# Kernel optimization log

Measured on AMD Instinct MI355X. Metric: run time of the kernel, lower is better.

## Reference

```python
import jax, jax.numpy as jnp
import numpy as np

B, S, D, H = 4, 2048, 1024, 16
HD = D // H  # 64

def setup_inputs() -> dict:
    key = jax.random.key(0)
    ks = jax.random.split(key, 6)
    scale = 1.0 / np.sqrt(D)
    return {
        "x": jax.random.normal(ks[0], (B, S, D), dtype=jnp.float32),
        "Wq": jax.random.normal(ks[1], (D, D), dtype=jnp.float32) * scale,
        "Wk": jax.random.normal(ks[2], (D, D), dtype=jnp.float32) * scale,
        "Wv": jax.random.normal(ks[3], (D, D), dtype=jnp.float32) * scale,
        "Wo": jax.random.normal(ks[4], (D, D), dtype=jnp.float32) * scale,
        "bo": jnp.zeros((D,), dtype=jnp.float32),
    }

def reference(x, Wq, Wk, Wv, Wo, bo):
    b, s, d = x.shape
    # projections (no bias for q/k/v, matching QKV_BIAS=False)
    q = (x @ Wq).reshape(b, s, H, HD).transpose(0, 2, 1, 3)  # [b,h,s,hd]
    k = (x @ Wk).reshape(b, s, H, HD).transpose(0, 2, 1, 3)
    v = (x @ Wv).reshape(b, s, H, HD).transpose(0, 2, 1, 3)
    scores = jnp.einsum('bhqd,bhkd->bhqk', q, k)  # [b,h,s,s]
    causal = jnp.tril(jnp.ones((s, s), dtype=bool))  # True where allowed
    scores = jnp.where(causal, scores, -jnp.inf)
    attn = jax.nn.softmax(scores / np.sqrt(HD), axis=-1)
    ctx = jnp.einsum('bhqk,bhkd->bhqd', attn, v)  # [b,h,s,hd]
    ctx = ctx.transpose(0, 2, 1, 3).reshape(b, s, d)
    return ctx @ Wo + bo
```

## Files before the change

kernel.cpp:

```cpp
#include <hip/hip_runtime.h>

#define BSZ 4
#define SEQ 2048
#define DIM 1024
#define NH  16
#define HD  64
#define QT  128
#define KT  64
#define PAD 72

typedef float v4f __attribute__((ext_vector_type(4)));
typedef short s8v __attribute__((ext_vector_type(8)));
typedef unsigned short u16;
typedef unsigned short u16x8 __attribute__((ext_vector_type(8)));
typedef unsigned short u16x4 __attribute__((ext_vector_type(4)));
typedef unsigned int u32;
typedef unsigned int u32x2 __attribute__((ext_vector_type(2)));
typedef unsigned int u32x4 __attribute__((ext_vector_type(4)));

__device__ __forceinline__ u16 f2bf(float f) {
  u32 u = __builtin_bit_cast(u32, f);
  u32 r = u + 0x7fffu + ((u >> 16) & 1u);
  return (u16)(r >> 16);
}
__device__ __forceinline__ u32 cvtpk(float lo, float hi) {
  u32 r; asm("v_cvt_pk_bf16_f32 %0, %1, %2" : "=v"(r) : "v"(lo), "v"(hi)); return r;
}
__device__ __forceinline__ u16 f2bf1(float f) { return (u16)cvtpk(f, f); }
__device__ __forceinline__ float fast_exp2(float x) {
#if __has_builtin(__builtin_amdgcn_exp2f)
  return __builtin_amdgcn_exp2f(x);
#else
  return exp2f(x);
#endif
}
__device__ __forceinline__ void gll16(const u16* g, u16* l) {
  __builtin_amdgcn_global_load_lds((const __attribute__((address_space(1))) void*)g,
                                   (__attribute__((address_space(3))) void*)l, 16, 0, 0);
}
__device__ __forceinline__ void wg_barrier() { asm volatile("s_barrier" ::: "memory"); }
#define WAITCNT_LGKM0 0xC07F
#define VMW8 __builtin_amdgcn_s_waitcnt(0xF78);
#define VMW6 __builtin_amdgcn_s_waitcnt(0xF76);
#define VMW4 __builtin_amdgcn_s_waitcnt(0xF74);
#define VMW0 __builtin_amdgcn_s_waitcnt(0xF70);
#define SCHEDB __builtin_amdgcn_sched_barrier(0);

__global__ __launch_bounds__(256) void cast_bf16_kernel(const float* __restrict__ x,
                                                        u16* __restrict__ o, int n4) {
  int i = blockIdx.x * 256 + threadIdx.x;
  if (i >= n4) return;
  v4f v = reinterpret_cast<const v4f*>(x)[i];
  u16x4 r;
  #pragma unroll
  for (int c = 0; c < 4; c++) r[c] = f2bf(v[c]);
  reinterpret_cast<u16x4*>(o)[i] = r;
}

__global__ __launch_bounds__(256) void transpose_cast_kernel(const float* __restrict__ W0,
                                                             const float* __restrict__ W1,
                                                             const float* __restrict__ W2,
                                                             const float* __restrict__ W3,
                                                             u16* __restrict__ out) {
  const float* W = blockIdx.z == 0 ? W0 : blockIdx.z == 1 ? W1 : blockIdx.z == 2 ? W2 : W3;
  const float scale = (blockIdx.z == 0) ? 0.18033688011112042f : 1.0f;
  u16* T = out + (size_t)blockIdx.z * DIM * DIM;
  __shared__ float tile[32][33];
  int tx = threadIdx.x & 31, ty = threadIdx.x >> 5;
  int bn = blockIdx.x * 32, bk = blockIdx.y * 32;
  #pragma unroll
  for (int r = 0; r < 4; r++) {
    int k = bk + ty + r * 8;
    tile[ty + r * 8][tx] = W[(size_t)k * DIM + bn + tx];
  }
  __syncthreads();
  #pragma unroll
  for (int r = 0; r < 4; r++) {
    int n = bn + ty + r * 8;
    T[(size_t)n * DIM + bk + tx] = f2bf(tile[tx][ty + r * 8] * scale);
  }
}


#define QST_A(t_, kc_, d_)                                                        \
  gll16(AgLo + (t_) * 64 + (kc_) * 32, ALw + (d_) * 16384 + (kc_) * 8192);        \
  gll16(AgHi + (t_) * 64 + (kc_) * 32, ALw + (d_) * 16384 + (kc_) * 8192 + 4096);
#define QST_B(t_, kc_, d_)                                                        \
  gll16(BgLo + (t_) * 64 + (kc_) * 32, BLw + (d_) * 16384 + (kc_) * 8192);        \
  gll16(BgHi + (t_) * 64 + (kc_) * 32, BLw + (d_) * 16384 + (kc_) * 8192 + 4096);

#define QRDB(d_, kc_)                                                             \
  bfr[0] = *(const s8v*)(BL + (d_) * 16384 + (kc_) * 8192 + (wn * 4 + 0) * 512 + rdo); \
  bfr[1] = *(const s8v*)(BL + (d_) * 16384 + (kc_) * 8192 + (wn * 4 + 1) * 512 + rdo); \
  bfr[2] = *(const s8v*)(BL + (d_) * 16384 + (kc_) * 8192 + (wn * 4 + 2) * 512 + rdo); \
  bfr[3] = *(const s8v*)(BL + (d_) * 16384 + (kc_) * 8192 + (wn * 4 + 3) * 512 + rdo);

#define QPH(d_, kc_, mh_, RDB_, STG_, VMW_)                                       \
  { _Pragma("unroll") for (int i_ = 0; i_ < 4; i_++)                              \
      afr[i_] = *(const s8v*)(AL + (d_) * 16384 + (kc_) * 8192 +                  \
                              (wm * 8 + (mh_) * 4 + i_) * 512 + rdo);             \
    RDB_                                                                          \
    STG_                                                                          \
    SCHEDB                                                                        \
    VMW_                                                                          \
    wg_barrier();                                                                 \
    __builtin_amdgcn_s_waitcnt(WAITCNT_LGKM0);                                    \
    SCHEDB                                                                        \
    __builtin_amdgcn_s_setprio(1);                                                \
    _Pragma("unroll") for (int i_ = 0; i_ < 4; i_++)                              \
      _Pragma("unroll") for (int j_ = 0; j_ < 4; j_++)                            \
        acc[(mh_) * 4 + i_][j_] = __builtin_amdgcn_mfma_f32_16x16x32_bf16(        \
            afr[i_], bfr[j_], acc[(mh_) * 4 + i_][j_], 0, 0, 0);                  \
    __builtin_amdgcn_s_setprio(0);                                                \
    wg_barrier(); }

__global__ __launch_bounds__(512, 2) void gemm_qkv(const u16* __restrict__ A, const u16* __restrict__ Wt,
                                                   u16* __restrict__ Qb, u16* __restrict__ Kb,
                                                   u16* __restrict__ Vtg) {
  const int bid = blockIdx.x;
  const int swz = (bid & 7) * 48 + (bid >> 3);
  const int z = swz >> 7;
  const int rem = swz & 127;
  const int m0 = (rem >> 2) * 256;
  const int n0 = (rem & 3) * 256;
  const u16* Bt = Wt + (size_t)z * DIM * DIM;

  extern __shared__ __align__(16) u16 lds[];
  const int t = threadIdx.x;
  const int lane = t & 63, w = t >> 6;
  const int wm = w >> 2, wn = w & 3;
  const int quad = lane >> 4, l16 = lane & 15;
  const int sR = lane & 15, sC = lane >> 4;
  u16* AL = lds;
  u16* BL = lds + 32768;
  u16* ALw = AL + w * 512;
  u16* BLw = BL + w * 512;
  const int rdo = quad * 128 + l16 * 8;
  const u16* AgLo = A + (size_t)(m0 + w * 16 + sR) * DIM + sC * 8;
  const u16* AgHi = AgLo + (size_t)128 * DIM;
  const u16* BgLo = Bt + (size_t)(n0 + w * 16 + sR) * DIM + sC * 8;
  const u16* BgHi = BgLo + (size_t)128 * DIM;

  v4f acc[8][4];
  #pragma unroll
  for (int i = 0; i < 8; i++)
    #pragma unroll
    for (int j = 0; j < 4; j++) acc[i][j] = (v4f){0.f, 0.f, 0.f, 0.f};
  s8v afr[4], bfr[4];

  QST_A(0, 0, 0) QST_B(0, 0, 0) QST_A(0, 1, 0) QST_B(0, 1, 0)
  QST_A(1, 0, 1) QST_B(1, 0, 1)
  SCHEDB
  VMW8
  wg_barrier();

  for (int it = 0; it < 7; ++it) {
    const int kt = it * 2;
    QPH(0, 0, 0, QRDB(0, 0), QST_A(kt + 1, 1, 1), )
    QPH(0, 0, 1, ,           QST_B(kt + 1, 1, 1), VMW6)
    QPH(0, 1, 0, QRDB(0, 1), QST_A(kt + 2, 0, 0), )
    QPH(0, 1, 1, ,           QST_B(kt + 2, 0, 0), VMW6)
    QPH(1, 0, 0, QRDB(1, 0), QST_A(kt + 2, 1, 0), )
    QPH(1, 0, 1, ,           QST_B(kt + 2, 1, 0), VMW6)
    QPH(1, 1, 0, QRDB(1, 1), QST_A(kt + 3, 0, 1), )
    QPH(1, 1, 1, ,           QST_B(kt + 3, 0, 1), VMW6)
  }
  QPH(0, 0, 0, QRDB(0, 0), QST_A(15, 1, 1), )
  QPH(0, 0, 1, ,           QST_B(15, 1, 1), VMW6)
  QPH(0, 1, 0, QRDB(0, 1), , )
  QPH(0, 1, 1, ,           , VMW4)
  QPH(1, 0, 0, QRDB(1, 0), , )
  QPH(1, 0, 1, ,           , VMW0)
  QPH(1, 1, 0, QRDB(1, 1), , )
  QPH(1, 1, 1, ,           , )

  if (z == 2) {
    #pragma unroll
    for (int mi = 0; mi < 8; mi++) {
      #pragma unroll
      for (int ni = 0; ni < 4; ni++) {
        int gm0 = m0 + wm * 128 + mi * 16 + quad * 4;
        int gn = n0 + wn * 64 + ni * 16 + l16;
        int b = gm0 >> 11, s0 = gm0 & (SEQ - 1), hh = gn >> 6, d = gn & (HD - 1);
        u32x2 pw;
        pw[0] = cvtpk(acc[mi][ni][0], acc[mi][ni][1]);
        pw[1] = cvtpk(acc[mi][ni][2], acc[mi][ni][3]);
        *(u16x4*)(Vtg + ((size_t)(b * NH + hh) * HD + d) * SEQ + s0) =
            __builtin_bit_cast(u16x4, pw);
      }
    }
  } else {
    u16* C = (z == 0) ? Qb : Kb;
    #pragma unroll
    for (int mi = 0; mi < 8; mi++) {
      #pragma unroll
      for (int ni = 0; ni < 4; ni++) {
        int gn = n0 + wn * 64 + ni * 16 + l16;
        #pragma unroll
        for (int r = 0; r < 4; r++) {
          int gm = m0 + wm * 128 + mi * 16 + quad * 4 + r;
          C[(size_t)gm * DIM + gn] = f2bf1(acc[mi][ni][r]);
        }
      }
    }
  }
}

#define ST_TILE(t_, s_)                                                           \
  gll16(Ag0 + (t_) * 64,      AW0 + (s_) * 16384);                                \
  gll16(Ag1 + (t_) * 64,      AW1 + (s_) * 16384);                                \
  gll16(Ag0 + (t_) * 64 + 32, AW0 + (s_) * 16384 + 8192);                         \
  gll16(Ag1 + (t_) * 64 + 32, AW1 + (s_) * 16384 + 8192);                         \
  gll16(Bg0 + (t_) * 64,      BW0 + (s_) * 8192);                                 \
  gll16(Bg0 + (t_) * 64 + 32, BW0 + (s_) * 8192 + 4096);

#define PH(t_, s_, STAGES, VMW)                                                   \
  { const u16* Ab = AL + (s_) * 16384 + aRd;                                      \
    const u16* Bb = BL + (s_) * 8192 + bRd;                                       \
    s8v af[2][4], bf[2][4];                                                       \
    _Pragma("unroll") for (int kc_ = 0; kc_ < 2; kc_++) {                         \
      _Pragma("unroll") for (int i_ = 0; i_ < 4; i_++)                            \
        af[kc_][i_] = *(const s8v*)(Ab + kc_ * 8192 + i_ * 512);                  \
      _Pragma("unroll") for (int j_ = 0; j_ < 4; j_++)                            \
        bf[kc_][j_] = *(const s8v*)(Bb + kc_ * 4096 + j_ * 512);                  \
    }                                                                             \
    STAGES                                                                        \
    VMW                                                                           \
    wg_barrier();                                                                 \
    __builtin_amdgcn_s_waitcnt(WAITCNT_LGKM0);                                    \
    __builtin_amdgcn_s_setprio(1);                                                \
    _Pragma("unroll") for (int kc_ = 0; kc_ < 2; kc_++)                           \
      _Pragma("unroll") for (int i_ = 0; i_ < 4; i_++)                            \
        _Pragma("unroll") for (int j_ = 0; j_ < 4; j_++)                          \
          acc[i_][j_] = __builtin_amdgcn_mfma_f32_16x16x32_bf16(                  \
              af[kc_][i_], bf[kc_][j_], acc[i_][j_], 0, 0, 0);                    \
    __builtin_amdgcn_s_setprio(0);                                                \
    wg_barrier(); }

__global__ __launch_bounds__(512, 2) void gemm_proj(const u16* __restrict__ A, const u16* __restrict__ Bt,
                                                    float* __restrict__ Cf, const float* __restrict__ bias) {
  const int bid = blockIdx.x;
  const int swz = (bid & 7) * 32 + (bid >> 3);
  const int m0 = (swz >> 3) * 256;
  const int n0 = (swz & 7) * 128;
  extern __shared__ __align__(16) u16 lds[];
  const int t = threadIdx.x;
  const int lane = t & 63, w = t >> 6;
  const int waveM = w >> 1, waveN = w & 1;
  const int quad = lane >> 4, l16 = lane & 15;
  const int sR = lane & 15, sC = lane >> 4;
  u16* AL = lds;
  u16* BL = lds + 49152;
  v4f acc[4][4];
  #pragma unroll
  for (int i = 0; i < 4; i++)
    #pragma unroll
    for (int j = 0; j < 4; j++) acc[i][j] = (v4f){0.f, 0.f, 0.f, 0.f};
  const u16* Ag0 = A + (size_t)(m0 + w * 32 + sR) * DIM + sC * 8;
  const u16* Ag1 = Ag0 + 16 * DIM;
  const u16* Bg0 = Bt + (size_t)(n0 + w * 16 + sR) * DIM + sC * 8;
  u16* AW0 = AL + w * 1024;
  u16* AW1 = AL + w * 1024 + 512;
  u16* BW0 = BL + w * 512;
  const int aRd = waveM * 2048 + quad * 128 + l16 * 8;
  const int bRd = waveN * 2048 + quad * 128 + l16 * 8;
  ST_TILE(0, 0) ST_TILE(1, 1)
  VMW6
  wg_barrier();
  #pragma unroll
  for (int t3 = 0; t3 < 12; t3 += 3) {
    PH(t3 + 0, 0, ST_TILE(t3 + 2, 2), VMW6)
    PH(t3 + 1, 1, ST_TILE(t3 + 3, 0), VMW6)
    PH(t3 + 2, 2, ST_TILE(t3 + 4, 1), VMW6)
  }
  PH(12, 0, ST_TILE(14, 2), VMW6)
  PH(13, 1, ST_TILE(15, 0), VMW6)
  PH(14, 2, , VMW0)
  PH(15, 0, , )
  #pragma unroll
  for (int ni = 0; ni < 4; ni++) {
    int gn = n0 + waveN * 64 + ni * 16 + l16;
    float bv = bias[gn];
    #pragma unroll
    for (int mi = 0; mi < 4; mi++) {
      #pragma unroll
      for (int r = 0; r < 4; r++) {
        int gm = m0 + waveM * 64 + mi * 16 + quad * 4 + r;
        Cf[(size_t)gm * DIM + gn] = acc[mi][ni][r] + bv;
      }
    }
  }
}

__global__ __launch_bounds__(256, 3) void flash_attn_mfma(const u16* __restrict__ Qb,
                                                          const u16* __restrict__ Kb,
                                                          const u16* __restrict__ Vtg,
                                                          u16* __restrict__ Ob) {
  const int h = blockIdx.x, px = blockIdx.y, bb = blockIdx.z;
  const int t = threadIdx.x;
  const int lane = t & 63, w = t >> 6;
  const int quad = lane >> 4, l16 = lane & 15;

  __shared__ u16 QPs[QT * PAD];
  __shared__ u16 Ks[KT * PAD];
  __shared__ u16 Vs[HD * PAD];

  const size_t qkbase = (size_t)bb * SEQ * DIM + h * HD;
  const size_t vbase = ((size_t)bb * NH + h) * (size_t)HD * SEQ;

  const int vrow = t >> 2, scol = (t & 3) * 16;
  const int krow = ((vrow >> 5) + 2 * ((vrow >> 2) & 1)) * 16 + ((vrow >> 3) & 3) * 4 + (vrow & 3);

  for (int pass = 0; pass < 2; pass++) {
    const int qi = (pass == 0) ? px : (SEQ / QT - 1 - px);
    const int q0 = qi * QT;
    const int wq = q0 + w * 32;
    const int ntiles = 2 * qi + 2;

    __syncthreads();

    {
      const int r = t >> 1, c0 = (t & 1) * 32;
      const u16* src = Qb + qkbase + (size_t)(q0 + r) * DIM + c0;
      #pragma unroll
      for (int ch = 0; ch < 4; ch++)
        *(u16x8*)(QPs + r * PAD + c0 + ch * 8) = *(const u16x8*)(src + ch * 8);
    }
    __syncthreads();

    s8v qf[2][2];
    #pragma unroll
    for (int ni = 0; ni < 2; ni++)
      #pragma unroll
      for (int kc = 0; kc < 2; kc++)
        qf[ni][kc] = *(const s8v*)(QPs + (w * 32 + ni * 16 + l16) * PAD + kc * 32 + quad * 8);

    u16x8 kr0, kr1, vr0, vr1;
    {
      const u16* kp = Kb + qkbase + (size_t)vrow * DIM + scol;
      kr0 = *(const u16x8*)kp; kr1 = *(const u16x8*)(kp + 8);
      const u16* vp = Vtg + vbase + (size_t)vrow * SEQ + scol;
      vr0 = *(const u16x8*)vp; vr1 = *(const u16x8*)(vp + 8);
    }

    float mrun[2] = {-1e30f, -1e30f}, lrun[2] = {0.f, 0.f};
    v4f O[4][2];
    #pragma unroll
    for (int di = 0; di < 4; di++)
      #pragma unroll
      for (int ni = 0; ni < 2; ni++) O[di][ni] = (v4f){0.f, 0.f, 0.f, 0.f};

    for (int it = 0; it < ntiles; ++it) {
      const int kv0 = it * KT;
      __syncthreads();
      *(u16x8*)(Ks + krow * PAD + scol) = kr0;
      *(u16x8*)(Ks + krow * PAD + scol + 8) = kr1;
      *(u16x8*)(Vs + vrow * PAD + scol) = vr0;
      *(u16x8*)(Vs + vrow * PAD + scol + 8) = vr1;
      __syncthreads();
      if (it + 1 < ntiles) {
        const int nkv = kv0 + KT;
        const u16* kp = Kb + qkbase + (size_t)(nkv + vrow) * DIM + scol;
        kr0 = *(const u16x8*)kp; kr1 = *(const u16x8*)(kp + 8);
        const u16* vp = Vtg + vbase + (size_t)vrow * SEQ + nkv + scol;
        vr0 = *(const u16x8*)vp; vr1 = *(const u16x8*)(vp + 8);
      }
      if (kv0 > wq + 31) continue;

      v4f sc[4][2];
      #pragma unroll
      for (int mi = 0; mi < 4; mi++)
        #pragma unroll
        for (int ni = 0; ni < 2; ni++) sc[mi][ni] = (v4f){0.f, 0.f, 0.f, 0.f};
      #pragma unroll
      for (int kc = 0; kc < 2; kc++) {
        #pragma unroll
        for (int mi = 0; mi < 4; mi++) {
          s8v kf = *(const s8v*)(Ks + (mi * 16 + l16) * PAD + kc * 32 + quad * 8);
          sc[mi][0] = __builtin_amdgcn_mfma_f32_16x16x32_bf16(kf, qf[0][kc], sc[mi][0], 0, 0, 0);
          sc[mi][1] = __builtin_amdgcn_mfma_f32_16x16x32_bf16(kf, qf[1][kc], sc[mi][1], 0, 0, 0);
        }
      }

      if (kv0 + KT > wq) {
        #pragma unroll
        for (int mi = 0; mi < 4; mi++) {
          const int kvb = kv0 + (mi & 1) * 32 + quad * 8 + (mi >> 1) * 4;
          #pragma unroll
          for (int ni = 0; ni < 2; ni++) {
            const int qg = wq + ni * 16 + l16;
            #pragma unroll
            for (int r = 0; r < 4; r++)
              if (kvb + r > qg) sc[mi][ni][r] = -1e30f;
          }
        }
      }

      float mx[2];
      #pragma unroll
      for (int ni = 0; ni < 2; ni++) {
        float m = -1e30f;
        #pragma unroll
        for (int mi = 0; mi < 4; mi++)
          #pragma unroll
          for (int r = 0; r < 4; r++) m = fmaxf(m, sc[mi][ni][r]);
        m = fmaxf(m, __shfl_xor(m, 16, 64));
        m = fmaxf(m, __shfl_xor(m, 32, 64));
        mx[ni] = m;
      }
      const bool defer = __all((mx[0] <= mrun[0] + 8.f) && (mx[1] <= mrun[1] + 8.f));
      if (!defer) {
        float alpha[2];
        #pragma unroll
        for (int ni = 0; ni < 2; ni++) {
          const float mnew = fmaxf(mrun[ni], mx[ni]);
          alpha[ni] = fast_exp2(mrun[ni] - mnew);
          mrun[ni] = mnew;
          lrun[ni] *= alpha[ni];
        }
        #pragma unroll
        for (int di = 0; di < 4; di++)
          #pragma unroll
          for (int ni = 0; ni < 2; ni++)
            #pragma unroll
            for (int r = 0; r < 4; r++) O[di][ni][r] *= alpha[ni];
      }
      #pragma unroll
      for (int ni = 0; ni < 2; ni++) {
        float rsum = 0.f;
        #pragma unroll
        for (int mi = 0; mi < 4; mi++)
          #pragma unroll
          for (int r = 0; r < 4; r++) {
            float p = fast_exp2(sc[mi][ni][r] - mrun[ni]);
            sc[mi][ni][r] = p;
            rsum += p;
          }
        rsum += __shfl_xor(rsum, 16, 64);
        rsum += __shfl_xor(rsum, 32, 64);
        lrun[ni] += rsum;
      }

      s8v pf[2][2];
      #pragma unroll
      for (int ni = 0; ni < 2; ni++)
        #pragma unroll
        for (int kc = 0; kc < 2; kc++) {
          u32x4 wds;
          wds[0] = cvtpk(sc[kc][ni][0], sc[kc][ni][1]);
          wds[1] = cvtpk(sc[kc][ni][2], sc[kc][ni][3]);
          wds[2] = cvtpk(sc[kc + 2][ni][0], sc[kc + 2][ni][1]);
          wds[3] = cvtpk(sc[kc + 2][ni][2], sc[kc + 2][ni][3]);
          pf[ni][kc] = __builtin_bit_cast(s8v, wds);
        }

      #pragma unroll
      for (int kc = 0; kc < 2; kc++) {
        #pragma unroll
        for (int di = 0; di < 4; di++) {
          s8v vf = *(const s8v*)(Vs + (di * 16 + l16) * PAD + kc * 32 + quad * 8);
          O[di][0] = __builtin_amdgcn_mfma_f32_16x16x32_bf16(vf, pf[0][kc], O[di][0], 0, 0, 0);
          O[di][1] = __builtin_amdgcn_mfma_f32_16x16x32_bf16(vf, pf[1][kc], O[di][1], 0, 0, 0);
        }
      }
    }

    const float inv0 = 1.f / lrun[0], inv1 = 1.f / lrun[1];
    #pragma unroll
    for (int di = 0; di < 4; di++)
      #pragma unroll
      for (int ni = 0; ni < 2; ni++) {
        const float inv = ni ? inv1 : inv0;
        #pragma unroll
        for (int r = 0; r < 4; r++)
          QPs[(w * 32 + ni * 16 + l16) * PAD + di * 16 + quad * 4 + r] = f2bf1(O[di][ni][r] * inv);
      }
    __syncthreads();
    {
      const int r = t >> 1, c0 = (t & 1) * 32;
      u16* dst = Ob + qkbase + (size_t)(q0 + r) * DIM + c0;
      #pragma unroll
      for (int ch = 0; ch < 4; ch++)
        *(u16x8*)(dst + ch * 8) = *(const u16x8*)(QPs + r * PAD + c0 + ch * 8);
    }
  }
}

extern "C" void kernel_launch(void* const* d_in, const int* in_sizes, int n_in,
                              void* d_out, int out_size, void* d_ws, size_t ws_size,
                              hipStream_t stream) {
  (void)in_sizes; (void)n_in; (void)out_size; (void)ws_size;
  const float* x  = (const float*)d_in[0];
  const float* Wq = (const float*)d_in[1];
  const float* Wk = (const float*)d_in[2];
  const float* Wv = (const float*)d_in[3];
  const float* Wo = (const float*)d_in[4];
  const float* bo = (const float*)d_in[5];
  float* out = (float*)d_out;

  static bool lds_attr_done = false;
  if (!lds_attr_done) {
    hipFuncSetAttribute(reinterpret_cast<const void*>(gemm_qkv),
                        hipFuncAttributeMaxDynamicSharedMemorySize, 131072);
    hipFuncSetAttribute(reinterpret_cast<const void*>(gemm_proj),
                        hipFuncAttributeMaxDynamicSharedMemorySize, 147456);
    lds_attr_done = true;
  }

  char* ws = (char*)d_ws;
  const size_t MB = 1024ull * 1024ull;
  u16* Xb  = (u16*)(ws);
  u16* Wt  = (u16*)(ws + 16 * MB);
  u16* Qb  = (u16*)(ws + 24 * MB);
  u16* Kb  = (u16*)(ws + 40 * MB);
  u16* Vtg = (u16*)(ws + 56 * MB);
  u16* Cb  = (u16*)(ws + 72 * MB);

  const int NTOK = BSZ * SEQ;
  const int n4 = NTOK * DIM / 4;
  cast_bf16_kernel<<<(n4 + 255) / 256, 256, 0, stream>>>(x, Xb, n4);
  transpose_cast_kernel<<<dim3(32, 32, 4), 256, 0, stream>>>(Wq, Wk, Wv, Wo, Wt);

  gemm_qkv<<<dim3(384), 512, 131072, stream>>>(Xb, Wt, Qb, Kb, Vtg);

  flash_attn_mfma<<<dim3(NH, SEQ / QT / 2, BSZ), 256, 0, stream>>>(Qb, Kb, Vtg, Cb);

  gemm_proj<<<dim3(256), 512, 147456, stream>>>(Cb, Wt + 3ull * DIM * DIM, out, bo);
}
```

Before: 266.6 us.

## Replace LDS-staged QKV GEMM with direct-global-load register double-buffered tiles

Rewrites the QKV projection GEMM so it no longer stages 256x256 tiles through LDS with an async global-to-LDS pipeline. It now uses 128x128 tiles, 256 threads and 1536 blocks, where each wave loads MFMA fragments straight from global memory into registers and double-buffers them. The goal is to drop LDS traffic and barriers and raise occupancy. In exchange, data reuse across waves is lost: each A and B fragment is fetched by several waves and the loads are strided row reads, so the kernel leans more on cache bandwidth.

```diff
diff --git a/kernel.cpp b/kernel.cpp
--- a/kernel.cpp
+++ b/kernel.cpp
@@ -40,11 +40,8 @@
 }
 __device__ __forceinline__ void wg_barrier() { asm volatile("s_barrier" ::: "memory"); }
 #define WAITCNT_LGKM0 0xC07F
-#define VMW8 __builtin_amdgcn_s_waitcnt(0xF78);
 #define VMW6 __builtin_amdgcn_s_waitcnt(0xF76);
-#define VMW4 __builtin_amdgcn_s_waitcnt(0xF74);
 #define VMW0 __builtin_amdgcn_s_waitcnt(0xF70);
-#define SCHEDB __builtin_amdgcn_sched_barrier(0);
 
 __global__ __launch_bounds__(256) void cast_bf16_kernel(const float* __restrict__ x,
                                                         u16* __restrict__ o, int n4) {
@@ -82,104 +79,64 @@
 }
 
 
-#define QST_A(t_, kc_, d_)                                                        \
-  gll16(AgLo + (t_) * 64 + (kc_) * 32, ALw + (d_) * 16384 + (kc_) * 8192);        \
-  gll16(AgHi + (t_) * 64 + (kc_) * 32, ALw + (d_) * 16384 + (kc_) * 8192 + 4096);
-#define QST_B(t_, kc_, d_)                                                        \
-  gll16(BgLo + (t_) * 64 + (kc_) * 32, BLw + (d_) * 16384 + (kc_) * 8192);        \
-  gll16(BgHi + (t_) * 64 + (kc_) * 32, BLw + (d_) * 16384 + (kc_) * 8192 + 4096);
-
-#define QRDB(d_, kc_)                                                             \
-  bfr[0] = *(const s8v*)(BL + (d_) * 16384 + (kc_) * 8192 + (wn * 4 + 0) * 512 + rdo); \
-  bfr[1] = *(const s8v*)(BL + (d_) * 16384 + (kc_) * 8192 + (wn * 4 + 1) * 512 + rdo); \
-  bfr[2] = *(const s8v*)(BL + (d_) * 16384 + (kc_) * 8192 + (wn * 4 + 2) * 512 + rdo); \
-  bfr[3] = *(const s8v*)(BL + (d_) * 16384 + (kc_) * 8192 + (wn * 4 + 3) * 512 + rdo);
-
-#define QPH(d_, kc_, mh_, RDB_, STG_, VMW_)                                       \
-  { _Pragma("unroll") for (int i_ = 0; i_ < 4; i_++)                              \
-      afr[i_] = *(const s8v*)(AL + (d_) * 16384 + (kc_) * 8192 +                  \
-                              (wm * 8 + (mh_) * 4 + i_) * 512 + rdo);             \
-    RDB_                                                                          \
-    STG_                                                                          \
-    SCHEDB                                                                        \
-    VMW_                                                                          \
-    wg_barrier();                                                                 \
-    __builtin_amdgcn_s_waitcnt(WAITCNT_LGKM0);                                    \
-    SCHEDB                                                                        \
-    __builtin_amdgcn_s_setprio(1);                                                \
-    _Pragma("unroll") for (int i_ = 0; i_ < 4; i_++)                              \
-      _Pragma("unroll") for (int j_ = 0; j_ < 4; j_++)                            \
-        acc[(mh_) * 4 + i_][j_] = __builtin_amdgcn_mfma_f32_16x16x32_bf16(        \
-            afr[i_], bfr[j_], acc[(mh_) * 4 + i_][j_], 0, 0, 0);                  \
-    __builtin_amdgcn_s_setprio(0);                                                \
-    wg_barrier(); }
-
-__global__ __launch_bounds__(512, 2) void gemm_qkv(const u16* __restrict__ A, const u16* __restrict__ Wt,
+#define QLOADS(AF, BF, K)                                                         \
+  AF[0] = *(const s8v*)(Ag0 + (K)); AF[1] = *(const s8v*)(Ag1 + (K));             \
+  AF[2] = *(const s8v*)(Ag2 + (K)); AF[3] = *(const s8v*)(Ag3 + (K));             \
+  BF[0] = *(const s8v*)(Bg0 + (K)); BF[1] = *(const s8v*)(Bg1 + (K));             \
+  BF[2] = *(const s8v*)(Bg2 + (K)); BF[3] = *(const s8v*)(Bg3 + (K));
+
+#define QMMS(AF, BF)                                                              \
+  _Pragma("unroll") for (int i_ = 0; i_ < 4; i_++)                                \
+    _Pragma("unroll") for (int j_ = 0; j_ < 4; j_++)                              \
+      acc[i_][j_] = __builtin_amdgcn_mfma_f32_16x16x32_bf16(                      \
+          AF[i_], BF[j_], acc[i_][j_], 0, 0, 0);
+
+__global__ __launch_bounds__(256, 3) void gemm_qkv(const u16* __restrict__ A, const u16* __restrict__ Wt,
                                                    u16* __restrict__ Qb, u16* __restrict__ Kb,
                                                    u16* __restrict__ Vtg) {
   const int bid = blockIdx.x;
-  const int swz = (bid & 7) * 48 + (bid >> 3);
-  const int z = swz >> 7;
-  const int rem = swz & 127;
-  const int m0 = (rem >> 2) * 256;
-  const int n0 = (rem & 3) * 256;
+  const int swz = (bid & 7) * 192 + (bid >> 3);
+  const int z = swz >> 9;
+  const int rem = swz & 511;
+  const int m0 = (rem >> 3) * 128;
+  const int n0 = (rem & 7) * 128;
   const u16* Bt = Wt + (size_t)z * DIM * DIM;
 
-  extern __shared__ __align__(16) u16 lds[];
   const int t = threadIdx.x;
   const int lane = t & 63, w = t >> 6;
-  const int wm = w >> 2, wn = w & 3;
+  const int wm = w >> 1, wn = w & 1;
   const int quad = lane >> 4, l16 = lane & 15;
-  const int sR = lane & 15, sC = lane >> 4;
-  u16* AL = lds;
-  u16* BL = lds + 32768;
-  u16* ALw = AL + w * 512;
-  u16* BLw = BL + w * 512;
-  const int rdo = quad * 128 + l16 * 8;
-  const u16* AgLo = A + (size_t)(m0 + w * 16 + sR) * DIM + sC * 8;
-  const u16* AgHi = AgLo + (size_t)128 * DIM;
-  const u16* BgLo = Bt + (size_t)(n0 + w * 16 + sR) * DIM + sC * 8;
-  const u16* BgHi = BgLo + (size_t)128 * DIM;
-
-  v4f acc[8][4];
-  #pragma unroll
-  for (int i = 0; i < 8; i++)
+
+  const u16* Ag0 = A + (size_t)(m0 + wm * 64 + 0 * 16 + l16) * DIM + quad * 8;
+  const u16* Ag1 = A + (size_t)(m0 + wm * 64 + 1 * 16 + l16) * DIM + quad * 8;
+  const u16* Ag2 = A + (size_t)(m0 + wm * 64 + 2 * 16 + l16) * DIM + quad * 8;
+  const u16* Ag3 = A + (size_t)(m0 + wm * 64 + 3 * 16 + l16) * DIM + quad * 8;
+  const u16* Bg0 = Bt + (size_t)(n0 + wn * 64 + 0 * 16 + l16) * DIM + quad * 8;
+  const u16* Bg1 = Bt + (size_t)(n0 + wn * 64 + 1 * 16 + l16) * DIM + quad * 8;
+  const u16* Bg2 = Bt + (size_t)(n0 + wn * 64 + 2 * 16 + l16) * DIM + quad * 8;
+  const u16* Bg3 = Bt + (size_t)(n0 + wn * 64 + 3 * 16 + l16) * DIM + quad * 8;
+
+  v4f acc[4][4];
+  #pragma unroll
+  for (int i = 0; i < 4; i++)
     #pragma unroll
     for (int j = 0; j < 4; j++) acc[i][j] = (v4f){0.f, 0.f, 0.f, 0.f};
-  s8v afr[4], bfr[4];
-
-  QST_A(0, 0, 0) QST_B(0, 0, 0) QST_A(0, 1, 0) QST_B(0, 1, 0)
-  QST_A(1, 0, 1) QST_B(1, 0, 1)
-  SCHEDB
-  VMW8
-  wg_barrier();
-
-  for (int it = 0; it < 7; ++it) {
-    const int kt = it * 2;
-    QPH(0, 0, 0, QRDB(0, 0), QST_A(kt + 1, 1, 1), )
-    QPH(0, 0, 1, ,           QST_B(kt + 1, 1, 1), VMW6)
-    QPH(0, 1, 0, QRDB(0, 1), QST_A(kt + 2, 0, 0), )
-    QPH(0, 1, 1, ,           QST_B(kt + 2, 0, 0), VMW6)
-    QPH(1, 0, 0, QRDB(1, 0), QST_A(kt + 2, 1, 0), )
-    QPH(1, 0, 1, ,           QST_B(kt + 2, 1, 0), VMW6)
-    QPH(1, 1, 0, QRDB(1, 1), QST_A(kt + 3, 0, 1), )
-    QPH(1, 1, 1, ,           QST_B(kt + 3, 0, 1), VMW6)
-  }
-  QPH(0, 0, 0, QRDB(0, 0), QST_A(15, 1, 1), )
-  QPH(0, 0, 1, ,           QST_B(15, 1, 1), VMW6)
-  QPH(0, 1, 0, QRDB(0, 1), , )
-  QPH(0, 1, 1, ,           , VMW4)
-  QPH(1, 0, 0, QRDB(1, 0), , )
-  QPH(1, 0, 1, ,           , VMW0)
-  QPH(1, 1, 0, QRDB(1, 1), , )
-  QPH(1, 1, 1, ,           , )
+
+  s8v afA[4], bfA[4], afB[4], bfB[4];
+  QLOADS(afA, bfA, 0)
+  #pragma unroll
+  for (int s = 0; s < 31; ++s) {
+    if ((s & 1) == 0) { QLOADS(afB, bfB, (s + 1) * 32) QMMS(afA, bfA) }
+    else              { QLOADS(afA, bfA, (s + 1) * 32) QMMS(afB, bfB) }
+  }
+  QMMS(afB, bfB)
 
   if (z == 2) {
     #pragma unroll
-    for (int mi = 0; mi < 8; mi++) {
+    for (int mi = 0; mi < 4; mi++) {
       #pragma unroll
       for (int ni = 0; ni < 4; ni++) {
-        int gm0 = m0 + wm * 128 + mi * 16 + quad * 4;
+        int gm0 = m0 + wm * 64 + mi * 16 + quad * 4;
         int gn = n0 + wn * 64 + ni * 16 + l16;
         int b = gm0 >> 11, s0 = gm0 & (SEQ - 1), hh = gn >> 6, d = gn & (HD - 1);
         u32x2 pw;
@@ -192,13 +149,13 @@
   } else {
     u16* C = (z == 0) ? Qb : Kb;
     #pragma unroll
-    for (int mi = 0; mi < 8; mi++) {
+    for (int mi = 0; mi < 4; mi++) {
       #pragma unroll
       for (int ni = 0; ni < 4; ni++) {
         int gn = n0 + wn * 64 + ni * 16 + l16;
         #pragma unroll
         for (int r = 0; r < 4; r++) {
-          int gm = m0 + wm * 128 + mi * 16 + quad * 4 + r;
+          int gm = m0 + wm * 64 + mi * 16 + quad * 4 + r;
           C[(size_t)gm * DIM + gn] = f2bf1(acc[mi][ni][r]);
         }
       }
@@ -500,8 +457,6 @@
 
   static bool lds_attr_done = false;
   if (!lds_attr_done) {
-    hipFuncSetAttribute(reinterpret_cast<const void*>(gemm_qkv),
-                        hipFuncAttributeMaxDynamicSharedMemorySize, 131072);
     hipFuncSetAttribute(reinterpret_cast<const void*>(gemm_proj),
                         hipFuncAttributeMaxDynamicSharedMemorySize, 147456);
     lds_attr_done = true;
@@ -521,7 +476,7 @@
   cast_bf16_kernel<<<(n4 + 255) / 256, 256, 0, stream>>>(x, Xb, n4);
   transpose_cast_kernel<<<dim3(32, 32, 4), 256, 0, stream>>>(Wq, Wk, Wv, Wo, Wt);
 
-  gemm_qkv<<<dim3(384), 512, 131072, stream>>>(Xb, Wt, Qb, Kb, Vtg);
+  gemm_qkv<<<dim3(1536), 256, 0, stream>>>(Xb, Wt, Qb, Kb, Vtg);
 
   flash_attn_mfma<<<dim3(NH, SEQ / QT / 2, BSZ), 256, 0, stream>>>(Qb, Kb, Vtg, Cb);
 
```

Measured after the change: 389.1 us. 45.9% more time.
